# Kernel tuning notes

Hardware: AMD Instinct MI355X
Metric: run time of the kernel (lower is better)

## Reference

```python
import jax, jax.numpy as jnp
import numpy as np

B, N, D, H = 64, 1025, 768, 128

def setup_inputs() -> dict:
    key = jax.random.key(0)
    ks = jax.random.split(key, 5)
    x = jax.random.normal(ks[0], (B, N, D), dtype=jnp.float32)
    ln_w = jnp.ones((D,), dtype=jnp.float32)
    ln_b = jnp.zeros((D,), dtype=jnp.float32)
    w1 = jax.random.normal(ks[1], (D, H), dtype=jnp.float32) * (1.0 / np.sqrt(D))
    b1 = jnp.zeros((H,), dtype=jnp.float32)
    w2 = jax.random.normal(ks[2], (H, 1), dtype=jnp.float32) * (1.0 / np.sqrt(H))
    b2 = jnp.zeros((1,), dtype=jnp.float32)
    return {"x": x, "ln_w": ln_w, "ln_b": ln_b, "w1": w1, "b1": b1, "w2": w2, "b2": b2, "k": 256}

def _layernorm(x, w, b, eps=1e-5):
    mu = jnp.mean(x, axis=-1, keepdims=True)
    var = jnp.mean(jnp.square(x - mu), axis=-1, keepdims=True)
    return (x - mu) * jax.lax.rsqrt(var + eps) * w + b

def reference(x, ln_w, ln_b, w1, b1, w2, b2, k):
    Bb, Nn, Dd = x.shape
    h = _layernorm(x, ln_w, ln_b)                      # [B,N,D]
    h = jax.nn.gelu(h @ w1 + b1, approximate=False)    # [B,N,H] (torch GELU = exact erf)
    scores = (h @ w2 + b2).squeeze(-1)                 # [B,N]
    scores = scores.at[:, 0].set(1e9)                  # force CLS kept
    kk = min(k, Nn - 1)
    patch_scores = scores[:, 1:]                       # [B,N-1]
    _, topk_idx = jax.lax.top_k(patch_scores, kk)      # [B,k]
    topk_idx = topk_idx + 1
    cls_idx = jnp.zeros((Bb, 1), dtype=topk_idx.dtype)
    idx_full = jnp.concatenate([cls_idx, topk_idx], axis=1)  # [B,1+k]
    x_reduced = jnp.take_along_axis(x, idx_full[:, :, None], axis=1)  # [B,1+k,D]
    return (x_reduced, idx_full, scores)
```

## Files before the change

### kernel.cpp

```cpp
#include <hip/hip_runtime.h>
#include <hip/hip_bf16.h>
#include <math.h>

#define BB 64
#define NN 1025
#define DD 768
#define HH 128
#define KK 256
#define TOK (BB*NN)
#define OUT_XRED 0
#define OUT_IDX  (BB*(KK+1)*DD)
#define OUT_SC   (OUT_IDX + BB*(KK+1))

typedef float    f32x4 __attribute__((ext_vector_type(4)));
typedef __fp16   h16x2 __attribute__((ext_vector_type(2)));
typedef _Float16 f16x8 __attribute__((ext_vector_type(8)));
#define NSTEP (DD/32)

union U4F { uint4 u; f16x8 h; };
union H2U { h16x2 h; unsigned int u; };

__global__ __launch_bounds__(256) void k_cvtw(const float* __restrict__ w1,
                                              const float* __restrict__ lnw,
                                              unsigned short* __restrict__ wt)
{
    int i = blockIdx.x*256 + threadIdx.x;
    int k = i >> 7, n = i & 127;
    union { _Float16 h; unsigned short s; } c;
    c.h = (_Float16)(w1[i] * lnw[k]);
    int s = k >> 5, g = (k >> 3) & 3, j = k & 7;
    wt[((s*4 + g)*HH + n)*8 + j] = c.s;
}

__global__ __launch_bounds__(128) void k_cvec(const float* __restrict__ w1,
                                              const float* __restrict__ lnw,
                                              const float* __restrict__ lnb,
                                              const float* __restrict__ b1,
                                              float* __restrict__ cvec)
{
    const int n = threadIdx.x;
    float s1 = 0.f, s2 = 0.f;
    #pragma unroll 8
    for (int k = 0; k < DD; ++k) {
        float wv = w1[k*HH + n];
        s1 = fmaf(lnb[k], wv, s1);
        s2 = fmaf(lnw[k], wv, s2);
    }
    cvec[n]      = s1 + b1[n];
    cvec[128+n]  = s2;
}

__global__ __launch_bounds__(256, 6) void k_fused(const float* __restrict__ x,
    const unsigned short* __restrict__ wt,
    const float* __restrict__ cvec,
    const float* __restrict__ w2, const float* __restrict__ b2,
    float* __restrict__ scores_out)
{
    __shared__ uint4 planes[16*96];
    __shared__ float mus[16], rss[16];
    __shared__ float part[4][16];

    const int tid  = threadIdx.x;
    const int wave = tid >> 6, lane = tid & 63;
    const int g    = lane >> 4, t16 = lane & 15;
    const int t7   = t16 & 7;
    const int tok0 = blockIdx.x * 16;
    const int colbase = wave * 32;
    const int row = tid >> 4, l16 = tid & 15;

    const float4* srow4 = reinterpret_cast<const float4*>(x + (size_t)(tok0 + row) * DD);
    const int rsz = row & 7;
    float s_ = 0.f, ss = 0.f;
    #pragma unroll
    for (int j = 0; j < 6; ++j) {
        float4 a = srow4[l16*2 + j*32];
        float4 b = srow4[l16*2 + j*32 + 1];
        s_ += ((a.x + a.y) + (a.z + a.w)) + ((b.x + b.y) + (b.z + b.w));
        ss += a.x*a.x + a.y*a.y + a.z*a.z + a.w*a.w
            + b.x*b.x + b.y*b.y + b.z*b.z + b.w*b.w;
        H2U h01, h23, h45, h67;
        h01.h = __builtin_amdgcn_cvt_pkrtz(a.x, a.y);
        h23.h = __builtin_amdgcn_cvt_pkrtz(a.z, a.w);
        h45.h = __builtin_amdgcn_cvt_pkrtz(b.x, b.y);
        h67.h = __builtin_amdgcn_cvt_pkrtz(b.z, b.w);
        planes[row*96 + ((l16 + j*16) ^ rsz)] = make_uint4(h01.u, h23.u, h45.u, h67.u);
    }
    #pragma unroll
    for (int m = 8; m; m >>= 1) { s_ += __shfl_xor(s_, m, 64); ss += __shfl_xor(ss, m, 64); }
    const float mu = s_ * (1.0f/768.0f);
    const float rs = 1.0f / sqrtf(ss * (1.0f/768.0f) - mu*mu + 1e-5f);
    if (l16 == 0) { mus[row] = mu; rss[row] = rs; }

    const unsigned short* wtp = wt + ((size_t)g*HH + colbase + t16)*8;
    f16x8 nB0 = *reinterpret_cast<const f16x8*>(wtp);
    f16x8 nB1 = *reinterpret_cast<const f16x8*>(wtp + 128);

    asm volatile("s_waitcnt lgkmcnt(0)" ::: "memory");
    __builtin_amdgcn_s_barrier();

    f32x4 acc0 = {0,0,0,0}, acc1 = {0,0,0,0};
    #pragma unroll
    for (int s = 0; s < NSTEP; ++s) {
        f16x8 B0 = nB0, B1 = nB1;
        if (s + 1 < NSTEP) {
            nB0 = *reinterpret_cast<const f16x8*>(wtp + (size_t)(s+1)*4096);
            nB1 = *reinterpret_cast<const f16x8*>(wtp + (size_t)(s+1)*4096 + 128);
        }
        U4F Ah;
        Ah.u = planes[((s*4 + g) ^ t7) + t16*96];
        acc0 = __builtin_amdgcn_mfma_f32_16x16x32_f16(Ah.h, B0, acc0, 0, 0, 0);
        acc1 = __builtin_amdgcn_mfma_f32_16x16x32_f16(Ah.h, B1, acc1, 0, 0, 0);
    }

    const int c0 = colbase + t16, c1i = colbase + 16 + t16;
    const float c1A = cvec[c0],      c2A = cvec[128 + c0];
    const float c1B = cvec[c1i],     c2B = cvec[128 + c1i];
    const float w2A = w2[c0],        w2B = w2[c1i];
    const float is2 = 0.70710678f;

    float psum[4];
    #pragma unroll
    for (int r = 0; r < 4; ++r) {
        const float mur = mus[g*4 + r], rsr = rss[g*4 + r];
        float v0 = rsr*acc0[r] + c1A - mur*rsr*c2A;
        float v1 = rsr*acc1[r] + c1B - mur*rsr*c2B;
        float g0 = 0.5f * v0 * (1.0f + erff(v0 * is2));
        float g1 = 0.5f * v1 * (1.0f + erff(v1 * is2));
        float p = g0 * w2A + g1 * w2B;
        #pragma unroll
        for (int m = 8; m; m >>= 1) p += __shfl_xor(p, m, 64);
        psum[r] = p;
    }
    if (t16 == 0) {
        #pragma unroll
        for (int r = 0; r < 4; ++r) part[wave][g*4 + r] = psum[r];
    }
    __syncthreads();
    if (tid < 16) {
        float s = part[0][tid] + part[1][tid] + part[2][tid] + part[3][tid] + b2[0];
        int tok = tok0 + tid;
        scores_out[tok] = ((tok % NN) == 0) ? 1.0e9f : s;
    }
}

__global__ __launch_bounds__(1024) void k_topk_gather(const float* __restrict__ scores,
                                                      const float* __restrict__ x,
                                                      float* __restrict__ idx_out,
                                                      float* __restrict__ xred)
{
    __shared__ float sk_[1024];
    __shared__ int   si[1024];
    const int tid = threadIdx.x;
    const int b   = blockIdx.x;
    sk_[tid] = scores[b*NN + 1 + tid];
    si[tid] = tid + 1;
    __syncthreads();
    for (int k = 2; k <= 1024; k <<= 1) {
        for (int j = k >> 1; j > 0; j >>= 1) {
            int ixj = tid ^ j;
            if (ixj > tid) {
                float sa = sk_[tid]; int ia = si[tid];
                float sb = sk_[ixj]; int ib = si[ixj];
                bool beforeB = (sb > sa) || (sb == sa && ib < ia);
                bool dirAsc  = ((tid & k) == 0);
                if (beforeB == dirAsc) {
                    sk_[tid] = sb; si[tid] = ib;
                    sk_[ixj] = sa; si[ixj] = ia;
                }
            }
            __syncthreads();
        }
    }
    if (tid == 0)  idx_out[b*(KK+1)] = 0.0f;
    if (tid < KK)  idx_out[b*(KK+1) + 1 + tid] = (float)si[tid];

    const float4* xb4 = reinterpret_cast<const float4*>(x + (size_t)b*NN*DD);
    float4* dst4 = reinterpret_cast<float4*>(xred + (size_t)b*(KK+1)*DD);
    for (int i = tid; i < (KK+1)*192; i += 1024) {
        int r = i / 192, c = i - r*192;
        int idx = (r == 0) ? 0 : si[r-1];
        dst4[i] = xb4[idx*192 + c];
    }
}

extern "C" void kernel_launch(void* const* d_in, const int* in_sizes, int n_in,
                              void* d_out, int out_size, void* d_ws, size_t ws_size,
                              hipStream_t stream)
{
    const float* x   = (const float*)d_in[0];
    const float* lnw = (const float*)d_in[1];
    const float* lnb = (const float*)d_in[2];
    const float* w1  = (const float*)d_in[3];
    const float* b1  = (const float*)d_in[4];
    const float* w2  = (const float*)d_in[5];
    const float* b2  = (const float*)d_in[6];

    float* out   = (float*)d_out;
    float* xred  = out + OUT_XRED;
    float* idxf  = out + OUT_IDX;
    float* scout = out + OUT_SC;

    unsigned short* wt = (unsigned short*)d_ws;
    float* cvec = (float*)((char*)d_ws + 196608);

    k_cvtw <<<DD*HH/256, 256, 0, stream>>>(w1, lnw, wt);
    k_cvec <<<1, 128, 0, stream>>>(w1, lnw, lnb, b1, cvec);
    k_fused<<<TOK/16, 256, 0, stream>>>(x, wt, cvec, w2, b2, scout);
    k_topk_gather<<<BB, 1024, 0, stream>>>(scout, x, idxf, xred);
}
```

Before: 118.5 us.

## Split top-k and gather into separate kernels and parallelize cvec reduction

The gather of selected rows moves out of the 64-block top-k kernel into its own kernel with one block per output row, so the copy runs across many more workgroups. The cvec precompute now uses 1024 threads with a shared-memory reduction instead of 128 threads each walking all 768 rows serially. The occupancy hint on the fused kernel is also dropped. The extra launch adds overhead and index reading via float conversion, and removing the occupancy hint may change register allocation.

```diff
diff --git a/kernel.cpp b/kernel.cpp
--- a/kernel.cpp
+++ b/kernel.cpp
@@ -32,25 +32,36 @@
     wt[((s*4 + g)*HH + n)*8 + j] = c.s;
 }
 
-__global__ __launch_bounds__(128) void k_cvec(const float* __restrict__ w1,
-                                              const float* __restrict__ lnw,
-                                              const float* __restrict__ lnb,
-                                              const float* __restrict__ b1,
-                                              float* __restrict__ cvec)
-{
-    const int n = threadIdx.x;
+__global__ __launch_bounds__(1024) void k_cvec(const float* __restrict__ w1,
+                                               const float* __restrict__ lnw,
+                                               const float* __restrict__ lnb,
+                                               const float* __restrict__ b1,
+                                               float* __restrict__ cvec)
+{
+    __shared__ float red[2][8][128];
+    const int n = threadIdx.x & 127;
+    const int r = threadIdx.x >> 7;
     float s1 = 0.f, s2 = 0.f;
     #pragma unroll 8
-    for (int k = 0; k < DD; ++k) {
+    for (int j = 0; j < 96; ++j) {
+        int k = r + j*8;
         float wv = w1[k*HH + n];
         s1 = fmaf(lnb[k], wv, s1);
         s2 = fmaf(lnw[k], wv, s2);
     }
-    cvec[n]      = s1 + b1[n];
-    cvec[128+n]  = s2;
-}
-
-__global__ __launch_bounds__(256, 6) void k_fused(const float* __restrict__ x,
+    red[0][r][n] = s1;
+    red[1][r][n] = s2;
+    __syncthreads();
+    if (r == 0) {
+        float t1 = 0.f, t2 = 0.f;
+        #pragma unroll
+        for (int q = 0; q < 8; ++q) { t1 += red[0][q][n]; t2 += red[1][q][n]; }
+        cvec[n]     = t1 + b1[n];
+        cvec[128+n] = t2;
+    }
+}
+
+__global__ __launch_bounds__(256) void k_fused(const float* __restrict__ x,
     const unsigned short* __restrict__ wt,
     const float* __restrict__ cvec,
     const float* __restrict__ w2, const float* __restrict__ b2,
@@ -143,10 +154,8 @@
     }
 }
 
-__global__ __launch_bounds__(1024) void k_topk_gather(const float* __restrict__ scores,
-                                                      const float* __restrict__ x,
-                                                      float* __restrict__ idx_out,
-                                                      float* __restrict__ xred)
+__global__ __launch_bounds__(1024) void k_topk(const float* __restrict__ scores,
+                                               float* __restrict__ idx_out)
 {
     __shared__ float sk_[1024];
     __shared__ int   si[1024];
@@ -173,14 +182,18 @@
     }
     if (tid == 0)  idx_out[b*(KK+1)] = 0.0f;
     if (tid < KK)  idx_out[b*(KK+1) + 1 + tid] = (float)si[tid];
-
-    const float4* xb4 = reinterpret_cast<const float4*>(x + (size_t)b*NN*DD);
-    float4* dst4 = reinterpret_cast<float4*>(xred + (size_t)b*(KK+1)*DD);
-    for (int i = tid; i < (KK+1)*192; i += 1024) {
-        int r = i / 192, c = i - r*192;
-        int idx = (r == 0) ? 0 : si[r-1];
-        dst4[i] = xb4[idx*192 + c];
-    }
+}
+
+__global__ __launch_bounds__(192) void k_gather(const float* __restrict__ x,
+                                                const float* __restrict__ idx_out,
+                                                float* __restrict__ xred)
+{
+    const int r = blockIdx.x;
+    const int b = r / (KK+1);
+    const int idx = (int)(idx_out[r] + 0.5f);
+    const float4* src = reinterpret_cast<const float4*>(x + ((size_t)b*NN + idx) * DD);
+    float4* dst = reinterpret_cast<float4*>(xred + (size_t)r * DD);
+    dst[threadIdx.x] = src[threadIdx.x];
 }
 
 extern "C" void kernel_launch(void* const* d_in, const int* in_sizes, int n_in,
@@ -204,7 +217,8 @@
     float* cvec = (float*)((char*)d_ws + 196608);
 
     k_cvtw <<<DD*HH/256, 256, 0, stream>>>(w1, lnw, wt);
-    k_cvec <<<1, 128, 0, stream>>>(w1, lnw, lnb, b1, cvec);
+    k_cvec <<<1, 1024, 0, stream>>>(w1, lnw, lnb, b1, cvec);
     k_fused<<<TOK/16, 256, 0, stream>>>(x, wt, cvec, w2, b2, scout);
-    k_topk_gather<<<BB, 1024, 0, stream>>>(scout, x, idxf, xred);
-}
+    k_topk <<<BB, 1024, 0, stream>>>(scout, idxf);
+    k_gather<<<BB*(KK+1), 192, 0, stream>>>(x, idxf, xred);
+}
```

Result: faster. 95.34 us (-19.5%).
